# Optimization experiments

Hardware: AMD Instinct MI355X
Metric: run time of the kernel (lower is better)

## Reference

```python
import jax, jax.numpy as jnp
import numpy as np

B, L, S = 128, 80, 8          # dialogues, utterances per dialogue, speakers
NODE_DIM, HIDDEN, HEADS, OUT_DIM = 768, 512, 8, 256
N = B * L


def _build_edges():
    """Replicates InterSentenceGNN.build_graph + Batch.from_data_list offsets."""
    rel = np.zeros((N, 3), np.float32)
    all_e, last = [], []
    eye3 = np.eye(3, dtype=np.float32)
    for b in range(B):
        off = b * L
        u = L - 1
        e, t = [], []
        for i in range(L):
            if i > 0:
                e += [[i - 1, i], [i, i - 1]]; t += [0, 0]   # REL_SEQ
            if i < u:
                e += [[i, u], [u, i]]; t += [1, 1]           # REL_CTX
        for s in range(S):                                   # REL_SPK, round-robin speakers
            g = list(range(s, L, S))
            for a in range(len(g)):
                for c in range(a + 1, len(g)):
                    e += [[g[a], g[c]], [g[c], g[a]]]; t += [2, 2]
        e = np.asarray(e, np.int64); t = np.asarray(t, np.int64)
        np.add.at(rel, e[:, 0] + off, eye3[t])               # out-degree per relation (pre-unique)
        all_e.append(np.unique(e, axis=0) + off)             # torch.unique(idx, dim=1)
        last.append(off + u)
    edge_index = np.concatenate(all_e, 0).T.astype(np.int32)  # [2, E], row0=src, row1=dst
    return edge_index, rel, np.asarray(last, np.int32)


def setup_inputs() -> dict:
    key = jax.random.key(0)
    ks = jax.random.split(key, 16)
    edge_index, rel_feat, last_idx = _build_edges()
    g = lambda k, shp, fan: jax.random.normal(k, shp, jnp.float32) * (1.0 / np.sqrt(fan))
    return {
        "x": jax.random.normal(ks[0], (N, NODE_DIM), jnp.float32),
        "rel_feat": jnp.asarray(rel_feat),
        "w1": g(ks[1], (3, 64), 3), "b1": jnp.zeros((64,), jnp.float32),
        "w2": g(ks[2], (64, 1), 64), "b2": jnp.zeros((1,), jnp.float32),
        "Wl1": g(ks[3], (NODE_DIM, HIDDEN), NODE_DIM), "bl1": jnp.zeros((HIDDEN,), jnp.float32),
        "Wr1": g(ks[4], (NODE_DIM, HIDDEN), NODE_DIM), "br1": jnp.zeros((HIDDEN,), jnp.float32),
        "att1": g(ks[5], (HEADS, HIDDEN // HEADS), HIDDEN // HEADS),
        "bias1": jnp.zeros((HIDDEN,), jnp.float32),
        "Wl2": g(ks[6], (HIDDEN, OUT_DIM), HIDDEN), "bl2": jnp.zeros((OUT_DIM,), jnp.float32),
        "Wr2": g(ks[7], (HIDDEN, OUT_DIM), HIDDEN), "br2": jnp.zeros((OUT_DIM,), jnp.float32),
        "att2": g(ks[8], (1, OUT_DIM), OUT_DIM),
        "bias2": jnp.zeros((OUT_DIM,), jnp.float32),
        "ln_g": jnp.ones((OUT_DIM,), jnp.float32), "ln_b": jnp.zeros((OUT_DIM,), jnp.float32),
        "edge_index": jnp.asarray(edge_index),
        "last_idx": jnp.asarray(last_idx),
    }


def _gatv2(x, Wl, bl, Wr, br, att, bias, src, dst, heads, ch, concat):
    """PyG GATv2Conv (eval mode, self-loops already in src/dst)."""
    n = x.shape[0]
    xl = (x @ Wl + bl).reshape(n, heads, ch)   # source transform (messages)
    xr = (x @ Wr + br).reshape(n, heads, ch)   # target transform
    e = jax.nn.leaky_relu(xl[src] + xr[dst], negative_slope=0.2)  # [E,H,C]
    logit = jnp.einsum("ehc,hc->eh", e, att)                      # [E,H]
    m = jax.ops.segment_max(logit, dst, num_segments=n)
    a = jnp.exp(logit - m[dst])
    denom = jax.ops.segment_sum(a, dst, num_segments=n)
    alpha = a / denom[dst]                                        # segment softmax over dst
    msg = (xl[src] * alpha[:, :, None]).reshape(-1, heads * ch)
    out = jax.ops.segment_sum(msg, dst, num_segments=n).reshape(n, heads, ch)
    out = out.reshape(n, heads * ch) if concat else out.mean(axis=1)
    return out + bias


def reference(x, rel_feat, w1, b1, w2, b2, Wl1, bl1, Wr1, br1, att1, bias1,
              Wl2, bl2, Wr2, br2, att2, bias2, ln_g, ln_b, edge_index, last_idx):
    n = x.shape[0]
    loops = jnp.arange(n, dtype=edge_index.dtype)
    src = jnp.concatenate([edge_index[0], loops])  # add_self_loops=True (PyG default)
    dst = jnp.concatenate([edge_index[1], loops])
    w = jax.nn.sigmoid(jax.nn.relu(rel_feat @ w1 + b1) @ w2 + b2)  # [N,1] node gate
    h = x * w
    h = jax.nn.elu(_gatv2(h, Wl1, bl1, Wr1, br1, att1, bias1, src, dst, HEADS, HIDDEN // HEADS, True))
    h = _gatv2(h, Wl2, bl2, Wr2, br2, att2, bias2, src, dst, 1, OUT_DIM, False)
    mu = jnp.mean(h, axis=-1, keepdims=True)
    var = jnp.mean((h - mu) ** 2, axis=-1, keepdims=True)
    h = (h - mu) * jax.lax.rsqrt(var + 1e-5) * ln_g + ln_b
    return h[last_idx]  # x[batch.ptr[1:] - 1]: last (context) node per dialogue
```

## Files before the change

### kernel.cpp

```cpp
#include <hip/hip_runtime.h>
#include <hip/hip_bf16.h>

#define NN 10240
#define LL 80
#define BB 128

typedef _Float16 half8 __attribute__((ext_vector_type(8)));
typedef _Float16 half2v __attribute__((ext_vector_type(2)));
typedef float f32x4 __attribute__((ext_vector_type(4)));

#define GLD16(gptr, lptr)                                                        \
  __builtin_amdgcn_global_load_lds(                                              \
      (const __attribute__((address_space(1))) void*)(gptr),                     \
      (__attribute__((address_space(3))) void*)(lptr), 16, 0, 0)

__device__ __forceinline__ float dot2f(half2v a, half2v b, float c) {
#if __has_builtin(__builtin_amdgcn_fdot2)
  return __builtin_amdgcn_fdot2(a, b, c, false);
#else
  return c + (float)a.x * (float)b.x + (float)a.y * (float)b.y;
#endif
}
__device__ __forceinline__ half2v u2h(unsigned int u) { half2v r; __builtin_memcpy(&r, &u, 4); return r; }
__device__ __forceinline__ unsigned int h2u(half2v h) { unsigned int u; __builtin_memcpy(&u, &h, 4); return u; }
__device__ __forceinline__ int roff(int r) { return r * 72; }

__device__ __forceinline__ float dotq4r(uint4 a, uint4 b, const half2v* atv, int qb, float acc) {
  const half2v c02 = {(_Float16)0.2f, (_Float16)0.2f};
  unsigned int aa[4] = {a.x, a.y, a.z, a.w};
  unsigned int bb[4] = {b.x, b.y, b.z, b.w};
#pragma unroll
  for (int j = 0; j < 4; ++j) {
    half2v e = u2h(aa[j]) + u2h(bb[j]);
    half2v l = __builtin_elementwise_max(e, e * c02);
    acc = dot2f(l, atv[qb + j], acc);
  }
  return acc;
}

__global__ __launch_bounds__(256) void prep_all(
    const float* __restrict__ x, const float* __restrict__ rel,
    const float* __restrict__ w1, const float* __restrict__ b1,
    const float* __restrict__ w2, const float* __restrict__ b2,
    const float* __restrict__ Wl1, const float* __restrict__ Wr1,
    const float* __restrict__ Wl2, const float* __restrict__ Wr2,
    const float* __restrict__ bl1, const float* __restrict__ br1,
    const float* __restrict__ att1,
    _Float16* __restrict__ h0, _Float16* __restrict__ Wt1,
    _Float16* __restrict__ Wt2cat,
    float* __restrict__ biasc, _Float16* __restrict__ att_h) {
  __shared__ float tile[32][33];
  int bid = blockIdx.x;
  int tid = threadIdx.x;
  if (bid < NN) {
    int n = bid;
    __shared__ float s_w;
    if (tid < 64) {
      float r0 = rel[n * 3 + 0], r1 = rel[n * 3 + 1], r2 = rel[n * 3 + 2];
      float v = r0 * w1[tid] + r1 * w1[64 + tid] + r2 * w1[128 + tid] + b1[tid];
      v = v > 0.f ? v : 0.f;
      v *= w2[tid];
      for (int d = 32; d; d >>= 1) v += __shfl_down(v, d, 64);
      if (tid == 0) s_w = 1.f / (1.f + __expf(-(v + b2[0])));
    }
    __syncthreads();
    float w = s_w;
    const float* xr = x + (size_t)n * 768;
    _Float16* hr = h0 + (size_t)n * 768;
    for (int c = tid; c < 768; c += 256) hr[c] = (_Float16)(xr[c] * w);
    return;
  }
  int r = bid - NN;
  const float* W;
  _Float16* Wt;
  int K, Nc, bx, by;
  if (r < 384)      { W = Wl1; Wt = Wt1;                          K = 768; Nc = 512; bx = r % 16;       by = r / 16; }
  else if (r < 768) { W = Wr1; Wt = Wt1 + (size_t)512 * 768;      K = 768; Nc = 512; bx = (r-384) % 16; by = (r-384) / 16; }
  else if (r < 896) { W = Wl2; Wt = Wt2cat;                       K = 512; Nc = 256; bx = (r-768) % 8;  by = (r-768) / 8; }
  else if (r < 1024){ W = Wr2; Wt = Wt2cat + (size_t)256 * 512;   K = 512; Nc = 256; bx = (r-896) % 8;  by = (r-896) / 8; }
  else {
    for (int i = tid; i < 1024; i += 256) biasc[i] = (i < 512) ? bl1[i] : br1[i - 512];
    for (int i = tid; i < 512; i += 256) att_h[i] = (_Float16)att1[i];
    return;
  }
  int n0 = bx * 32, k0 = by * 32;
  int c = tid & 31, rr = tid >> 5;
#pragma unroll
  for (int p = 0; p < 4; ++p) {
    int rw = p * 8 + rr;
    tile[rw][c] = W[(size_t)(k0 + rw) * Nc + n0 + c];
  }
  __syncthreads();
#pragma unroll
  for (int p = 0; p < 4; ++p) {
    int rw = p * 8 + rr;
    Wt[(size_t)(n0 + rw) * K + k0 + c] = (_Float16)tile[c][rw];
  }
}

__global__ __launch_bounds__(512, 6) void gemm1gat1(
    const _Float16* __restrict__ h0, const _Float16* __restrict__ Wt1,
    const float* __restrict__ biasc, const _Float16* __restrict__ att_h,
    const float* __restrict__ bias1, _Float16* __restrict__ h1) {
  __shared__ __align__(16) char smem[53248];
  _Float16* Ab = (_Float16*)smem;
  _Float16* Bb = (_Float16*)(smem + 20480);
  _Float16* s_xl = (_Float16*)smem;
  _Float16* s_xr = (_Float16*)(smem + 11520);
  float* s_logit = (float*)(smem + 23040);
  signed char* s_src8 = (signed char*)(smem + 27200);
  float* s_hub = (float*)(smem + 28240);
  _Float16* s_xlT = (_Float16*)(smem + 28560);
  _Float16* s_P = (_Float16*)smem;

  int bx = blockIdx.x;
  int h = bx >> 7, b = bx & 127;
  int base = b * LL;
  int tid = threadIdx.x;
  int wave = tid >> 6, lane = tid & 63;
  int lr = lane & 15, lk = lane >> 4;

  int segA8 = ((lane & 7) ^ ((lane >> 3) & 7)) * 8;
  int r0a = wave * 16 + (lane >> 3);
  const _Float16* aP0 = h0;
  const _Float16* aP1 = h0;
  if (wave < 5) {
    aP0 = h0 + (size_t)(base + r0a) * 768 + segA8;
    aP1 = h0 + (size_t)(base + r0a + 8) * 768 + segA8;
  }
  int rb0 = r0a, rb1 = r0a + 8;
  int wr0 = (rb0 < 64) ? (h * 64 + rb0) : (512 + h * 64 + (rb0 - 64));
  int wr1 = (rb1 < 64) ? (h * 64 + rb1) : (512 + h * 64 + (rb1 - 64));
  const _Float16* bP0 = Wt1 + (size_t)wr0 * 768 + segA8;
  const _Float16* bP1 = Wt1 + (size_t)wr1 * 768 + segA8;

  f32x4 acc[5] = {};
  if (wave < 5) {
    GLD16(aP0, Ab + wave * 1024);
    GLD16(aP1, Ab + wave * 1024 + 512);
  }
  GLD16(bP0, Bb + wave * 1024);
  GLD16(bP1, Bb + wave * 1024 + 512);
  __syncthreads();
  for (int t = 0; t < 12; ++t) {
    int cur = t & 1;
    if (t < 11) {
      int k0 = (t + 1) * 64;
      int nb = cur ^ 1;
      if (wave < 5) {
        GLD16(aP0 + k0, Ab + nb * 5120 + wave * 1024);
        GLD16(aP1 + k0, Ab + nb * 5120 + wave * 1024 + 512);
      }
      GLD16(bP0 + k0, Bb + nb * 8192 + wave * 1024);
      GLD16(bP1 + k0, Bb + nb * 8192 + wave * 1024 + 512);
    }
    const _Float16* Ac = Ab + cur * 5120;
    const _Float16* Bc = Bb + cur * 8192;
    int rB = wave * 16 + lr;
#pragma unroll
    for (int s2 = 0; s2 < 2; ++s2) {
      int cx = ((s2 * 4 + lk) ^ (lr & 7)) * 8;
      half8 bf = *(const half8*)(Bc + rB * 64 + cx);
#pragma unroll
      for (int m = 0; m < 5; ++m) {
        half8 af = *(const half8*)(Ac + (m * 16 + lr) * 64 + cx);
        acc[m] = __builtin_amdgcn_mfma_f32_16x16x32_f16(af, bf, acc[m], 0, 0, 0);
      }
    }
    __syncthreads();
  }
  {
    int c = wave * 16 + lr;
    bool isxl = c < 64;
    int cc = isxl ? c : c - 64;
    float bb = biasc[(isxl ? 0 : 512) + h * 64 + cc];
    _Float16* dst = isxl ? s_xl : s_xr;
#pragma unroll
    for (int m = 0; m < 5; ++m)
#pragma unroll
      for (int rg = 0; rg < 4; ++rg) {
        int row = m * 16 + lk * 4 + rg;
        _Float16 hv = (_Float16)(acc[m][rg] + bb);
        dst[roff(row) + cc] = hv;
        if (isxl) s_xlT[cc * 88 + row] = hv;
      }
  }
  if (tid < 79) {
    int d = tid;
    signed char list[13];
    int c = 0;
    list[c++] = (signed char)d;
    if (d > 0) list[c++] = (signed char)(d - 1);
    if (d + 1 < 79) list[c++] = (signed char)(d + 1);
    list[c++] = 79;
    for (int j = d & 7; j < 80; j += 8)
      if (j != d && j != 79) list[c++] = (signed char)j;
    for (int i = c; i < 13; ++i) list[i] = -1;
#pragma unroll
    for (int i = 0; i < 13; ++i) s_src8[i * 80 + d] = list[i];
  }
  __syncthreads();

  const unsigned int* pat = (const unsigned int*)(att_h + h * 64);
  half2v atv[32];
#pragma unroll
  for (int q = 0; q < 32; ++q) atv[q] = u2h(__builtin_amdgcn_readfirstlane(pat[q]));
  if (tid < 474) {
    int d = tid / 6, io = tid % 6;
    const uint4* pxr = (const uint4*)(s_xr + roff(d));
    uint4 xrr[8];
#pragma unroll
    for (int q = 0; q < 8; ++q) xrr[q] = pxr[q];
#pragma unroll
    for (int k = 0; k < 3; ++k) {
      int i = io + 6 * k;
      if (i < 13) {
        int src = s_src8[i * 80 + d];
        if (src < 0) {
          s_logit[i * 80 + d] = -3e38f;
        } else {
          const uint4* pxl = (const uint4*)(s_xl + roff(src));
          float a2 = 0.f;
#pragma unroll
          for (int q = 0; q < 8; ++q) a2 = dotq4r(pxl[q], xrr[q], atv, q * 4, a2);
          s_logit[i * 80 + d] = a2;
        }
      }
    }
  } else {
    int j = tid - 474;
    const uint4* pxr = (const uint4*)(s_xr + roff(79));
    uint4 xrr[8];
#pragma unroll
    for (int q = 0; q < 8; ++q) xrr[q] = pxr[q];
#pragma unroll
    for (int k = 0; k < 3; ++k) {
      int s = j + 38 * k;
      if (s < 80) {
        const uint4* pxl = (const uint4*)(s_xl + roff(s));
        float a2 = 0.f;
#pragma unroll
        for (int q = 0; q < 8; ++q) a2 = dotq4r(pxl[q], xrr[q], atv, q * 4, a2);
        s_hub[s] = a2;
      }
    }
  }
  __syncthreads();

  {
    uint4 z4 = {0u, 0u, 0u, 0u};
    for (int z = tid; z < 1040; z += 512) ((uint4*)smem)[z] = z4;
  }
  float va[13], inv_d = 0.f;
  bool isd = tid < 79;
  if (isd) {
    int d = tid;
    float m = -3e38f;
#pragma unroll
    for (int i = 0; i < 13; ++i) { va[i] = s_logit[i * 80 + d]; m = fmaxf(m, va[i]); }
    float sum = 0.f;
#pragma unroll
    for (int i = 0; i < 13; ++i) { va[i] = __expf(va[i] - m); sum += va[i]; }
    inv_d = 1.f / sum;
  }
  float he0 = 0.f, he1 = 0.f, hinv = 0.f;
  if (wave == 7) {
    int l = lane;
    float v0 = s_hub[l];
    float v1 = (l < 16) ? s_hub[64 + l] : -3e38f;
    float m = fmaxf(v0, v1);
    for (int d = 32; d; d >>= 1) m = fmaxf(m, __shfl_xor(m, d, 64));
    he0 = __expf(v0 - m);
    he1 = (l < 16) ? __expf(v1 - m) : 0.f;
    float sum = he0 + he1;
    for (int d = 32; d; d >>= 1) sum += __shfl_xor(sum, d, 64);
    hinv = 1.f / sum;
  }
  __syncthreads();

  if (isd) {
    int d = tid;
#pragma unroll
    for (int i = 0; i < 13; ++i) {
      int src = s_src8[i * 80 + d];
      if (src >= 0) s_P[d * 104 + src] = (_Float16)(va[i] * inv_d);
    }
  }
  if (wave == 7) {
    int l = lane;
    s_P[79 * 104 + l] = (_Float16)(he0 * hinv);
    if (l < 16) s_P[79 * 104 + 64 + l] = (_Float16)(he1 * hinv);
  }
  __syncthreads();

  {
    int nt = (wave < 4) ? 3 : 2;
    int tb = (wave < 4) ? wave * 3 : 12 + (wave - 4) * 2;
    for (int tt = 0; tt < nt; ++tt) {
      int t = tb + tt;
      int m = t >> 2, n = t & 3;
      f32x4 a = {};
#pragma unroll
      for (int kc = 0; kc < 3; ++kc) {
        half8 af = *(const half8*)(s_P + (m * 16 + lr) * 104 + kc * 32 + lk * 8);
        half8 bf = *(const half8*)(s_xlT + (n * 16 + lr) * 88 + kc * 32 + lk * 8);
        a = __builtin_amdgcn_mfma_f32_16x16x32_f16(af, bf, a, 0, 0, 0);
      }
      int c = n * 16 + lr;
      float bb = bias1[h * 64 + c];
#pragma unroll
      for (int rg = 0; rg < 4; ++rg) {
        int d = m * 16 + lk * 4 + rg;
        float v = a[rg] + bb;
        v = v > 0.f ? v : __expf(v) - 1.f;
        h1[(size_t)(base + d) * 512 + h * 64 + c] = (_Float16)v;
      }
    }
  }
}

#define PX 266
__global__ __launch_bounds__(512) void gemm2gat2(
    const _Float16* __restrict__ h1, const _Float16* __restrict__ Bt,
    const float* __restrict__ bl2, const float* __restrict__ br2,
    const float* __restrict__ att2, const float* __restrict__ bias2,
    const float* __restrict__ ln_g, const float* __restrict__ ln_b,
    float* __restrict__ out) {
  __shared__ __align__(16) char smem[43008];
  __shared__ _Float16 s_att[256];
  __shared__ _Float16 s_xr[256];
  __shared__ float s_red[80];
  __shared__ float s_sum[4], s_sq[4];
  _Float16* Ab = (_Float16*)smem;
  _Float16* Bb = (_Float16*)(smem + 10240);
  _Float16* s_x = (_Float16*)smem;

  int b = blockIdx.x;
  int tid = threadIdx.x;
  int wave = tid >> 6, lane = tid & 63;
  int lr = lane & 15, lk = lane >> 4;

  if (tid < 256) s_att[tid] = (_Float16)att2[tid];

  int seg8 = ((lane & 3) ^ ((lane >> 3) & 3)) * 8;
  int achunk = wave * 64 + lane;
  const _Float16* aP = h1 + (size_t)(b * 80 + (achunk >> 2)) * 512 + seg8;
  const _Float16* bP0 = Bt + (size_t)((wave * 128 + lane) >> 2) * 512 + seg8;
  const _Float16* bP1 = Bt + (size_t)((wave * 128 + 64 + lane) >> 2) * 512 + seg8;
  int xk8 = (lk ^ ((lr >> 1) & 3)) * 8;
  f32x4 acc[5][2] = {};
  if (wave < 5) GLD16(aP, Ab + wave * 512);
  GLD16(bP0, Bb + wave * 1024);
  GLD16(bP1, Bb + wave * 1024 + 512);
  __syncthreads();
  for (int t = 0; t < 16; ++t) {
    int cur = t & 1;
    if (t < 15) {
      int k0 = (t + 1) * 32;
      int nb = cur ^ 1;
      if (wave < 5) GLD16(aP + k0, Ab + nb * 2560 + wave * 512);
      GLD16(bP0 + k0, Bb + nb * 8192 + wave * 1024);
      GLD16(bP1 + k0, Bb + nb * 8192 + wave * 1024 + 512);
    }
    const _Float16* Ac = Ab + cur * 2560;
    const _Float16* Bc = Bb + cur * 8192;
    half8 af[5];
#pragma unroll
    for (int i = 0; i < 5; ++i)
      af[i] = *(const half8*)(Ac + (i * 16 + lr) * 32 + xk8);
#pragma unroll
    for (int j = 0; j < 2; ++j) {
      half8 bfv = *(const half8*)(Bc + ((wave * 2 + j) * 16 + lr) * 32 + xk8);
#pragma unroll
      for (int i = 0; i < 5; ++i)
        acc[i][j] = __builtin_amdgcn_mfma_f32_16x16x32_f16(af[i], bfv, acc[i][j], 0, 0, 0);
    }
    __syncthreads();
  }
#pragma unroll
  for (int i = 0; i < 5; ++i)
#pragma unroll
    for (int j = 0; j < 2; ++j)
#pragma unroll
      for (int rg = 0; rg < 4; ++rg) {
        int row = i * 16 + lk * 4 + rg;
        int col = (wave * 2 + j) * 16 + lr;
        s_x[row * PX + col] = (_Float16)(acc[i][j][rg] + bl2[col]);
      }
  {
    int c = tid >> 1, kh = tid & 1;
    const uint4* wr = (const uint4*)(Bt + (size_t)(256 + c) * 512 + kh * 256);
    const uint4* hq = (const uint4*)(h1 + (size_t)(b * 80 + 79) * 512 + kh * 256);
    float s = 0.f;
#pragma unroll 8
    for (int q = 0; q < 32; ++q) {
      uint4 ua = hq[q], uw = wr[q];
      s = dot2f(u2h(ua.x), u2h(uw.x), s);
      s = dot2f(u2h(ua.y), u2h(uw.y), s);
      s = dot2f(u2h(ua.z), u2h(uw.z), s);
      s = dot2f(u2h(ua.w), u2h(uw.w), s);
    }
    s += __shfl_xor(s, 1, 64);
    if (kh == 0) s_xr[c] = (_Float16)(s + br2[c]);
  }
  __syncthreads();
  if (tid < 160) {
    int r = tid >> 1, hf = tid & 1;
    const half2v* xa = (const half2v*)(s_x + r * PX + hf * 128);
    const half2v* xr = (const half2v*)(s_xr + hf * 128);
    const half2v* at = (const half2v*)(s_att + hf * 128);
    float lg = 0.f;
    const half2v c02 = {(_Float16)0.2f, (_Float16)0.2f};
#pragma unroll
    for (int q = 0; q < 64; ++q) {
      half2v e = xa[q] + xr[q];
      half2v l = __builtin_elementwise_max(e, e * c02);
      lg = dot2f(l, at[q], lg);
    }
    lg += __shfl_xor(lg, 1, 64);
    if (hf == 0) s_red[r] = lg;
  }
  __syncthreads();
  if (wave == 7) {
    float v0 = s_red[lane];
    float v1 = (lane < 16) ? s_red[64 + lane] : -3e38f;
    float m = fmaxf(v0, v1);
    for (int d = 32; d; d >>= 1) m = fmaxf(m, __shfl_xor(m, d, 64));
    float e0 = __expf(v0 - m);
    float e1 = (lane < 16) ? __expf(v1 - m) : 0.f;
    float sum = e0 + e1;
    for (int d = 32; d; d >>= 1) sum += __shfl_xor(sum, d, 64);
    float inv = 1.f / sum;
    s_red[lane] = e0 * inv;
    if (lane < 16) s_red[64 + lane] = e1 * inv;
  }
  __syncthreads();
  float v = 0.f;
  if (tid < 256) {
    float a = 0.f;
#pragma unroll
    for (int r = 0; r < 80; ++r) a += s_red[r] * (float)s_x[r * PX + tid];
    v = a + bias2[tid];
    float p = v;
    for (int d = 32; d; d >>= 1) p += __shfl_down(p, d, 64);
    if (lane == 0) s_sum[wave] = p;
    float q = v * v;
    for (int d = 32; d; d >>= 1) q += __shfl_down(q, d, 64);
    if (lane == 0) s_sq[wave] = q;
  }
  __syncthreads();
  if (tid < 256) {
    float mu = (s_sum[0] + s_sum[1] + s_sum[2] + s_sum[3]) * (1.f / 256.f);
    float ex2 = (s_sq[0] + s_sq[1] + s_sq[2] + s_sq[3]) * (1.f / 256.f);
    float var = ex2 - mu * mu;
    float r = rsqrtf(var + 1e-5f);
    out[b * 256 + tid] = (v - mu) * r * ln_g[tid] + ln_b[tid];
  }
}

extern "C" void kernel_launch(void* const* d_in, const int* in_sizes, int n_in,
                              void* d_out, int out_size, void* d_ws, size_t ws_size,
                              hipStream_t stream) {
  const float* x      = (const float*)d_in[0];
  const float* rel    = (const float*)d_in[1];
  const float* w1     = (const float*)d_in[2];
  const float* b1     = (const float*)d_in[3];
  const float* w2     = (const float*)d_in[4];
  const float* b2     = (const float*)d_in[5];
  const float* Wl1    = (const float*)d_in[6];
  const float* bl1    = (const float*)d_in[7];
  const float* Wr1    = (const float*)d_in[8];
  const float* br1    = (const float*)d_in[9];
  const float* att1   = (const float*)d_in[10];
  const float* bias1  = (const float*)d_in[11];
  const float* Wl2    = (const float*)d_in[12];
  const float* bl2    = (const float*)d_in[13];
  const float* Wr2    = (const float*)d_in[14];
  const float* br2    = (const float*)d_in[15];
  const float* att2   = (const float*)d_in[16];
  const float* bias2  = (const float*)d_in[17];
  const float* ln_g   = (const float*)d_in[18];
  const float* ln_b   = (const float*)d_in[19];
  float* out = (float*)d_out;

  char* p = (char*)d_ws;
  _Float16* h0     = (_Float16*)p; p += (size_t)NN * 768 * 2;
  _Float16* h1     = (_Float16*)p; p += (size_t)NN * 512 * 2;
  _Float16* Wt1    = (_Float16*)p; p += (size_t)1024 * 768 * 2;
  _Float16* Wt2cat = (_Float16*)p; p += (size_t)512 * 512 * 2;
  _Float16* att_h  = (_Float16*)p; p += 1024;
  float* biasc     = (float*)p; p += 1024 * 4;

  prep_all<<<NN + 1025, 256, 0, stream>>>(x, rel, w1, b1, w2, b2, Wl1, Wr1, Wl2, Wr2,
                                          bl1, br1, att1, h0, Wt1, Wt2cat, biasc, att_h);

  gemm1gat1<<<1024, 512, 0, stream>>>(h0, Wt1, biasc, att_h, bias1, h1);

  gemm2gat2<<<BB, 512, 0, stream>>>(h1, Wt2cat, bl2, br2, att2, bias2, ln_g, ln_b, out);
}
```

Baseline: 186.8 us.

## Split layer-2 GEMM into its own wide kernel and vectorize prep gating

The fused per-dialogue GEMM+GAT2 kernel ran only 128 blocks. The layer-2 xl GEMM now runs as a separate 640-block kernel writing an fp16 intermediate, and the GAT2+LayerNorm kernel reads it back, so more CUs work on the GEMM. The prep kernel also handles four nodes per block (one per wave) with float4 loads and packed half stores, and no longer needs shared memory or a block barrier. The cost is an extra launch and an extra round trip of the intermediate through global memory.

```diff
diff --git a/kernel.cpp b/kernel.cpp
--- a/kernel.cpp
+++ b/kernel.cpp
@@ -52,25 +52,30 @@
   __shared__ float tile[32][33];
   int bid = blockIdx.x;
   int tid = threadIdx.x;
-  if (bid < NN) {
-    int n = bid;
-    __shared__ float s_w;
-    if (tid < 64) {
-      float r0 = rel[n * 3 + 0], r1 = rel[n * 3 + 1], r2 = rel[n * 3 + 2];
-      float v = r0 * w1[tid] + r1 * w1[64 + tid] + r2 * w1[128 + tid] + b1[tid];
-      v = v > 0.f ? v : 0.f;
-      v *= w2[tid];
-      for (int d = 32; d; d >>= 1) v += __shfl_down(v, d, 64);
-      if (tid == 0) s_w = 1.f / (1.f + __expf(-(v + b2[0])));
-    }
-    __syncthreads();
-    float w = s_w;
-    const float* xr = x + (size_t)n * 768;
+  if (bid < 2560) {
+    int wave = tid >> 6, l = tid & 63;
+    int n = bid * 4 + wave;
+    float r0 = rel[n * 3 + 0], r1 = rel[n * 3 + 1], r2 = rel[n * 3 + 2];
+    float v = r0 * w1[l] + r1 * w1[64 + l] + r2 * w1[128 + l] + b1[l];
+    v = v > 0.f ? v : 0.f;
+    v *= w2[l];
+    for (int d = 32; d; d >>= 1) v += __shfl_down(v, d, 64);
+    float s = __shfl(v, 0, 64);
+    float g = 1.f / (1.f + __expf(-(s + b2[0])));
+    const float4* xr = (const float4*)(x + (size_t)n * 768);
     _Float16* hr = h0 + (size_t)n * 768;
-    for (int c = tid; c < 768; c += 256) hr[c] = (_Float16)(xr[c] * w);
+#pragma unroll
+    for (int i = 0; i < 3; ++i) {
+      int f = i * 64 + l;
+      float4 xv = xr[f];
+      half2v p0 = {(_Float16)(xv.x * g), (_Float16)(xv.y * g)};
+      half2v p1 = {(_Float16)(xv.z * g), (_Float16)(xv.w * g)};
+      uint2 ov = {h2u(p0), h2u(p1)};
+      *(uint2*)&hr[f * 4] = ov;
+    }
     return;
   }
-  int r = bid - NN;
+  int r = bid - 2560;
   const float* W;
   _Float16* Wt;
   int K, Nc, bx, by;
@@ -319,74 +324,78 @@
   }
 }
 
-#define PX 266
-__global__ __launch_bounds__(512) void gemm2gat2(
+__global__ __launch_bounds__(256) void gemm2a(
     const _Float16* __restrict__ h1, const _Float16* __restrict__ Bt,
-    const float* __restrict__ bl2, const float* __restrict__ br2,
+    const float* __restrict__ bl2, _Float16* __restrict__ xl2) {
+  __shared__ __align__(16) char smem[16384];
+  _Float16* Ab = (_Float16*)smem;
+  _Float16* Bb = (_Float16*)(smem + 8192);
+  int bx = blockIdx.x;
+  int mb = bx >> 2, nb = bx & 3;
+  int tid = threadIdx.x;
+  int wave = tid >> 6, lane = tid & 63;
+  int lr = lane & 15, lk = lane >> 4;
+  int seg8 = ((lane & 3) ^ ((lane >> 3) & 3)) * 8;
+  int row = tid >> 2;
+  const _Float16* aP = h1 + (size_t)(mb * 64 + row) * 512 + seg8;
+  const _Float16* bP = Bt + (size_t)(nb * 64 + row) * 512 + seg8;
+  int xk8 = (lk ^ ((lr >> 1) & 3)) * 8;
+  f32x4 acc[4] = {};
+  GLD16(aP, Ab + wave * 512);
+  GLD16(bP, Bb + wave * 512);
+  __syncthreads();
+  for (int t = 0; t < 16; ++t) {
+    int cur = t & 1;
+    if (t < 15) {
+      int k0 = (t + 1) * 32;
+      int nbuf = cur ^ 1;
+      GLD16(aP + k0, Ab + nbuf * 2048 + wave * 512);
+      GLD16(bP + k0, Bb + nbuf * 2048 + wave * 512);
+    }
+    const _Float16* Ac = Ab + cur * 2048;
+    const _Float16* Bc = Bb + cur * 2048;
+    half8 bf = *(const half8*)(Bc + (wave * 16 + lr) * 32 + xk8);
+#pragma unroll
+    for (int m = 0; m < 4; ++m) {
+      half8 af = *(const half8*)(Ac + (m * 16 + lr) * 32 + xk8);
+      acc[m] = __builtin_amdgcn_mfma_f32_16x16x32_f16(af, bf, acc[m], 0, 0, 0);
+    }
+    __syncthreads();
+  }
+  int col = nb * 64 + wave * 16 + lr;
+  float bb = bl2[col];
+#pragma unroll
+  for (int m = 0; m < 4; ++m)
+#pragma unroll
+    for (int rg = 0; rg < 4; ++rg) {
+      int r = mb * 64 + m * 16 + lk * 4 + rg;
+      xl2[(size_t)r * 256 + col] = (_Float16)(acc[m][rg] + bb);
+    }
+}
+
+#define PX 264
+__global__ __launch_bounds__(512) void gat2ln(
+    const _Float16* __restrict__ h1, const _Float16* __restrict__ xl2,
+    const _Float16* __restrict__ Bt, const float* __restrict__ br2,
     const float* __restrict__ att2, const float* __restrict__ bias2,
     const float* __restrict__ ln_g, const float* __restrict__ ln_b,
     float* __restrict__ out) {
-  __shared__ __align__(16) char smem[43008];
+  __shared__ __align__(16) _Float16 s_x[80 * PX];
   __shared__ _Float16 s_att[256];
   __shared__ _Float16 s_xr[256];
   __shared__ float s_red[80];
   __shared__ float s_sum[4], s_sq[4];
-  _Float16* Ab = (_Float16*)smem;
-  _Float16* Bb = (_Float16*)(smem + 10240);
-  _Float16* s_x = (_Float16*)smem;
 
   int b = blockIdx.x;
   int tid = threadIdx.x;
   int wave = tid >> 6, lane = tid & 63;
-  int lr = lane & 15, lk = lane >> 4;
 
   if (tid < 256) s_att[tid] = (_Float16)att2[tid];
-
-  int seg8 = ((lane & 3) ^ ((lane >> 3) & 3)) * 8;
-  int achunk = wave * 64 + lane;
-  const _Float16* aP = h1 + (size_t)(b * 80 + (achunk >> 2)) * 512 + seg8;
-  const _Float16* bP0 = Bt + (size_t)((wave * 128 + lane) >> 2) * 512 + seg8;
-  const _Float16* bP1 = Bt + (size_t)((wave * 128 + 64 + lane) >> 2) * 512 + seg8;
-  int xk8 = (lk ^ ((lr >> 1) & 3)) * 8;
-  f32x4 acc[5][2] = {};
-  if (wave < 5) GLD16(aP, Ab + wave * 512);
-  GLD16(bP0, Bb + wave * 1024);
-  GLD16(bP1, Bb + wave * 1024 + 512);
-  __syncthreads();
-  for (int t = 0; t < 16; ++t) {
-    int cur = t & 1;
-    if (t < 15) {
-      int k0 = (t + 1) * 32;
-      int nb = cur ^ 1;
-      if (wave < 5) GLD16(aP + k0, Ab + nb * 2560 + wave * 512);
-      GLD16(bP0 + k0, Bb + nb * 8192 + wave * 1024);
-      GLD16(bP1 + k0, Bb + nb * 8192 + wave * 1024 + 512);
-    }
-    const _Float16* Ac = Ab + cur * 2560;
-    const _Float16* Bc = Bb + cur * 8192;
-    half8 af[5];
-#pragma unroll
-    for (int i = 0; i < 5; ++i)
-      af[i] = *(const half8*)(Ac + (i * 16 + lr) * 32 + xk8);
-#pragma unroll
-    for (int j = 0; j < 2; ++j) {
-      half8 bfv = *(const half8*)(Bc + ((wave * 2 + j) * 16 + lr) * 32 + xk8);
-#pragma unroll
-      for (int i = 0; i < 5; ++i)
-        acc[i][j] = __builtin_amdgcn_mfma_f32_16x16x32_f16(af[i], bfv, acc[i][j], 0, 0, 0);
-    }
-    __syncthreads();
-  }
-#pragma unroll
-  for (int i = 0; i < 5; ++i)
-#pragma unroll
-    for (int j = 0; j < 2; ++j)
-#pragma unroll
-      for (int rg = 0; rg < 4; ++rg) {
-        int row = i * 16 + lk * 4 + rg;
-        int col = (wave * 2 + j) * 16 + lr;
-        s_x[row * PX + col] = (_Float16)(acc[i][j][rg] + bl2[col]);
-      }
+  for (int t = tid; t < 2560; t += 512) {
+    int row = t >> 5, q = t & 31;
+    uint4 v = *(const uint4*)(xl2 + ((size_t)(b * 80 + row)) * 256 + q * 8);
+    *(uint4*)(s_x + row * PX + q * 8) = v;
+  }
   {
     int c = tid >> 1, kh = tid & 1;
     const uint4* wr = (const uint4*)(Bt + (size_t)(256 + c) * 512 + kh * 256);
@@ -490,11 +499,14 @@
   _Float16* Wt2cat = (_Float16*)p; p += (size_t)512 * 512 * 2;
   _Float16* att_h  = (_Float16*)p; p += 1024;
   float* biasc     = (float*)p; p += 1024 * 4;
-
-  prep_all<<<NN + 1025, 256, 0, stream>>>(x, rel, w1, b1, w2, b2, Wl1, Wr1, Wl2, Wr2,
-                                          bl1, br1, att1, h0, Wt1, Wt2cat, biasc, att_h);
+  _Float16* xl2    = (_Float16*)p; p += (size_t)NN * 256 * 2;
+
+  prep_all<<<2560 + 1025, 256, 0, stream>>>(x, rel, w1, b1, w2, b2, Wl1, Wr1, Wl2, Wr2,
+                                            bl1, br1, att1, h0, Wt1, Wt2cat, biasc, att_h);
 
   gemm1gat1<<<1024, 512, 0, stream>>>(h0, Wt1, biasc, att_h, bias1, h1);
 
-  gemm2gat2<<<BB, 512, 0, stream>>>(h1, Wt2cat, bl2, br2, att2, bias2, ln_g, ln_b, out);
-}
+  gemm2a<<<640, 256, 0, stream>>>(h1, Wt2cat, bl2, xl2);
+
+  gat2ln<<<BB, 512, 0, stream>>>(h1, xl2, Wt2cat, br2, att2, bias2, ln_g, ln_b, out);
+}
```

New measurement: 179.8 us. 1.04x faster.
